# Optimization experiments

Hardware: AMD Instinct MI355X
Metric: run time of the kernel (lower is better)

The kernel has to match this reference:

```python
import jax, jax.numpy as jnp
import numpy as np

LAGS = 2
LATENT = 64          # latent_size; number of tiny per-dim MLPs
HID = 64             # hidden_dim of each MLP2
SLOPE = 0.2          # LeakyReLU negative slope
IN_DIM = LAGS * LATENT + 1  # 129: flattened lags + current value of dim i


def setup_inputs() -> dict:
    key = jax.random.key(0)
    k0, k1, k2, k3, k4 = jax.random.split(key, 5)
    B, LEN = 32, 512
    x = jax.random.normal(k0, (B, LEN + LAGS, LATENT), jnp.float32)
    # Stacked per-latent MLP2 params (num_layers=1):
    #   Linear(IN_DIM -> HID) + LeakyReLU(0.2) + Linear(HID -> 1)
    s1 = float(1.0 / np.sqrt(IN_DIM))
    s2 = float(1.0 / np.sqrt(HID))
    W1 = jax.random.uniform(k1, (LATENT, HID, IN_DIM), jnp.float32, -s1, s1)
    b1 = jax.random.uniform(k2, (LATENT, HID), jnp.float32, -s1, s1)
    W2 = jax.random.uniform(k3, (LATENT, HID), jnp.float32, -s2, s2)
    b2 = jax.random.uniform(k4, (LATENT,), jnp.float32, -s2, s2)
    return {"x": x, "W1": W1, "b1": b1, "W2": W2, "b2": b2}


def reference(x, W1, b1, W2, b2):
    B, T, xd = x.shape
    length = T - LAGS
    N = B * length
    # torch unfold(dim=1, size=LAGS+1, step=1).transpose(2,3) -> [B, length, LAGS+1, xd]
    idx = jnp.arange(length)[:, None] + jnp.arange(LAGS + 1)[None, :]
    win = x[:, idx]                                   # [B, length, LAGS+1, xd]
    lagsx = win[:, :, :-1].reshape(N, LAGS * xd)      # [N, LAGS*xd]
    xt = win[:, :, -1].reshape(N, xd)                 # [N, xd] current values per latent dim
    # gs[i] input = concat(lagsx, xt[:, i:i+1]); batch all latent dims at once.
    W1_lags = W1[:, :, :-1]                           # [L, H, LAGS*xd]
    w1_t = W1[:, :, -1]                               # [L, H] weight on the appended x_t column
    pre = (jnp.einsum('nd,lhd->nlh', lagsx, W1_lags)
           + xt[:, :, None] * w1_t[None]
           + b1[None])                                # [N, L, H]
    act = jnp.where(pre >= 0, pre, SLOPE * pre)       # LeakyReLU(0.2)
    residuals = jnp.einsum('nlh,lh->nl', act, W2) + b2[None]   # [N, L]
    # Analytic last column of the per-sample Jacobian (d residual_i / d x_t_i):
    dact = jnp.where(pre >= 0, 1.0, SLOPE)
    J_last = jnp.einsum('lh,nlh,lh->nl', W2, dact, w1_t)       # [N, L]
    logabsdet = jnp.sum(jnp.log(jnp.abs(J_last)), axis=-1)     # [N]
    return residuals.reshape(B, length, xd), logabsdet.reshape(B, length)
```

## Files before the change

kernel.cpp:

```cpp
#include <hip/hip_runtime.h>
#include <math.h>

#define SLOPE  0.2f
#define NB     32
#define LEN    512
#define LATENT 64
#define HID    64
#define IN_DIM 129
#define TROWS  514
#define NTOT   (NB * LEN)

typedef __attribute__((ext_vector_type(8)))  short bf16x8;
typedef __attribute__((ext_vector_type(16))) float f32x16;
typedef __attribute__((ext_vector_type(4)))  float f32x4;

struct alignas(8) US4 { unsigned short x, y, z, w; };

__device__ inline void bsplit(float v, unsigned short& hi, unsigned short& lo) {
    unsigned int u  = __builtin_bit_cast(unsigned int, v);
    unsigned int hb = (u + 0x7fffu + ((u >> 16) & 1u)) >> 16;
    hi = (unsigned short)hb;
    float fh = __builtin_bit_cast(float, hb << 16);
    float r  = v - fh;
    unsigned int u2 = __builtin_bit_cast(unsigned int, r);
    lo = (unsigned short)((u2 + 0x7fffu + ((u2 >> 16) & 1u)) >> 16);
}

__global__ __launch_bounds__(256)
void conv_w1(const float* __restrict__ W1g, unsigned short* __restrict__ W1f,
             float* __restrict__ W1t, float* __restrict__ out_lad) {
    const int idx = blockIdx.x * 256 + threadIdx.x;
    if (idx < NTOT) out_lad[idx] = 0.f;
    const int row  = idx >> 4;
    const int o    = idx & 15;
    const int ks   = o >> 1, hi32 = o & 1;
    const int l    = row >> 6, h = row & 63;
    const int i    = h >> 5,  r32 = h & 31;
    const int lane = hi32 * 32 + r32;
    const float* src = W1g + (size_t)row * IN_DIM + o * 8;
    unsigned short hh[8], ll[8];
    #pragma unroll
    for (int e = 0; e < 8; ++e) bsplit(src[e], hh[e], ll[e]);
    const size_t base = (size_t)l * 16384 + (size_t)i * 8192 + (size_t)ks * 1024
                      + (size_t)lane * 8;
    *reinterpret_cast<US4*>(W1f + base)       = US4{hh[0], hh[1], hh[2], hh[3]};
    *reinterpret_cast<US4*>(W1f + base + 4)   = US4{hh[4], hh[5], hh[6], hh[7]};
    *reinterpret_cast<US4*>(W1f + base + 512) = US4{ll[0], ll[1], ll[2], ll[3]};
    *reinterpret_cast<US4*>(W1f + base + 516) = US4{ll[4], ll[5], ll[6], ll[7]};
    if (o == 15) W1t[row] = src[8];
}

__global__ __launch_bounds__(512, 2)
void fused_mfma(const float* __restrict__ xg,
                const float* __restrict__ b1g, const float* __restrict__ W2g,
                const float* __restrict__ b2g,
                const unsigned short* __restrict__ W1f,
                const float* __restrict__ W1t,
                float* __restrict__ out_res, float* __restrict__ out_lad)
{
    __shared__ unsigned short sXh[66][72];
    __shared__ unsigned short sXl[66][72];
    __shared__ float sXt[66][8];
    __shared__ float sJ[64][8];
    __shared__ float sR[64][8];

    const int tid  = threadIdx.x;
    const int by   = blockIdx.x & 7;
    const int ht   = blockIdx.x >> 3;
    const int pt   = ht >> 1;
    const int s0   = (ht & 1) * 4;
    const int wn   = tid >> 6;
    const int lane = tid & 63;
    const int r32  = lane & 31;
    const int hi32 = lane >> 5;
    const int l    = by * 8 + wn;

    const unsigned short* A0 = W1f + (size_t)l * 16384 + (size_t)lane * 8;

    #pragma unroll 1
    for (int s = s0; s < s0 + 4; ++s) {
        const size_t xrow0 = (size_t)pt * TROWS + s * 64;

        for (int i = tid; i < 66 * 16; i += 512) {
            const int row = i >> 4, c4 = (i & 15) << 2;
            const float4 v = *reinterpret_cast<const float4*>(
                xg + (xrow0 + row) * LATENT + c4);
            unsigned short h0,h1,h2,h3, l0,l1,l2,l3;
            bsplit(v.x, h0, l0); bsplit(v.y, h1, l1);
            bsplit(v.z, h2, l2); bsplit(v.w, h3, l3);
            *reinterpret_cast<US4*>(&sXh[row][c4]) = US4{h0, h1, h2, h3};
            *reinterpret_cast<US4*>(&sXl[row][c4]) = US4{l0, l1, l2, l3};
        }
        for (int i = tid; i < 66 * 8; i += 512) {
            const int row = i >> 3, w = i & 7;
            sXt[row][w] = xg[(xrow0 + row) * LATENT + by * 8 + w];
        }
        __syncthreads();

        f32x16 acc[2][2];
        #pragma unroll
        for (int i = 0; i < 2; ++i)
            #pragma unroll
            for (int g = 0; g < 4; ++g) {
                const f32x4 b14 = *reinterpret_cast<const f32x4*>(
                    b1g + l * HID + i * 32 + hi32 * 4 + g * 8);
                #pragma unroll
                for (int m = 0; m < 4; ++m) {
                    acc[i][0][g * 4 + m] = b14[m];
                    acc[i][1][g * 4 + m] = b14[m];
                }
            }

        #pragma unroll
        for (int ks = 0; ks < 8; ++ks) {
            const int lag = ks >> 2;
            const int cc  = (ks & 3) * 16 + hi32 * 8;
            const unsigned short* p0 = A0 + ks * 1024;
            bf16x8 awh[2], awl[2], bxh[2], bxl[2];
            #pragma unroll
            for (int i = 0; i < 2; ++i) {
                awh[i] = *reinterpret_cast<const bf16x8*>(p0 + i * 8192);
                awl[i] = *reinterpret_cast<const bf16x8*>(p0 + i * 8192 + 512);
            }
            #pragma unroll
            for (int j = 0; j < 2; ++j) {
                const int rr = j * 32 + r32 + lag;
                bxh[j] = *reinterpret_cast<const bf16x8*>(&sXh[rr][cc]);
                bxl[j] = *reinterpret_cast<const bf16x8*>(&sXl[rr][cc]);
            }
            #pragma unroll
            for (int i = 0; i < 2; ++i)
                #pragma unroll
                for (int j = 0; j < 2; ++j) {
                    acc[i][j] = __builtin_amdgcn_mfma_f32_32x32x16_bf16(awh[i], bxh[j], acc[i][j], 0, 0, 0);
                    acc[i][j] = __builtin_amdgcn_mfma_f32_32x32x16_bf16(awh[i], bxl[j], acc[i][j], 0, 0, 0);
                    acc[i][j] = __builtin_amdgcn_mfma_f32_32x32x16_bf16(awl[i], bxh[j], acc[i][j], 0, 0, 0);
                }
        }

        const float xt0 = sXt[r32 + 2][wn];
        const float xt1 = sXt[32 + r32 + 2][wn];
        float res0 = 0.f, res1 = 0.f, jp0 = 0.f, jp1 = 0.f, jc = 0.f;

        #pragma unroll
        for (int i = 0; i < 2; ++i)
            #pragma unroll
            for (int g = 0; g < 4; ++g) {
                const int h0 = l * HID + i * 32 + hi32 * 4 + g * 8;
                const f32x4 wt = *reinterpret_cast<const f32x4*>(W1t + h0);
                const f32x4 w2 = *reinterpret_cast<const f32x4*>(W2g + h0);
                #pragma unroll
                for (int m = 0; m < 4; ++m) {
                    const float c0 = w2[m] * wt[m];
                    jc += c0;
                    const int r = g * 4 + m;
                    const float pre0 = fmaf(xt0, wt[m], acc[i][0][r]);
                    const float pre1 = fmaf(xt1, wt[m], acc[i][1][r]);
                    res0 += w2[m] * fmaxf(pre0, SLOPE * pre0);
                    res1 += w2[m] * fmaxf(pre1, SLOPE * pre1);
                    jp0 += (pre0 >= 0.f) ? c0 : 0.f;
                    jp1 += (pre1 >= 0.f) ? c0 : 0.f;
                }
            }

        res0 += __shfl_xor(res0, 32);
        res1 += __shfl_xor(res1, 32);
        jp0  += __shfl_xor(jp0, 32);
        jp1  += __shfl_xor(jp1, 32);
        jc   += __shfl_xor(jc, 32);

        if (hi32 == 0) {
            const float b2v = b2g[l];
            sR[r32][wn]      = res0 + b2v;
            sR[r32 + 32][wn] = res1 + b2v;
            sJ[r32][wn]      = SLOPE * jc + (1.f - SLOPE) * jp0;
            sJ[r32 + 32][wn] = SLOPE * jc + (1.f - SLOPE) * jp1;
        }
        __syncthreads();

        const size_t nbase = (size_t)pt * LEN + s * 64;
        if (tid < 128) {
            const int n = tid >> 1, part = (tid & 1) * 4;
            *reinterpret_cast<f32x4*>(out_res + (nbase + n) * LATENT + by * 8 + part) =
                *reinterpret_cast<const f32x4*>(&sR[n][part]);
        } else if (tid >= 448) {
            const int n = tid - 448;
            const float p = sJ[n][0] * sJ[n][1] * sJ[n][2] * sJ[n][3]
                          * sJ[n][4] * sJ[n][5] * sJ[n][6] * sJ[n][7];
            atomicAdd(&out_lad[nbase + n], logf(fabsf(p)));
        }
        __syncthreads();
    }
}

extern "C" void kernel_launch(void* const* d_in, const int* in_sizes, int n_in,
                              void* d_out, int out_size, void* d_ws, size_t ws_size,
                              hipStream_t stream) {
    const float* xg  = (const float*)d_in[0];
    const float* W1g = (const float*)d_in[1];
    const float* b1g = (const float*)d_in[2];
    const float* W2g = (const float*)d_in[3];
    const float* b2g = (const float*)d_in[4];

    float* out_res = (float*)d_out;
    float* out_lad = out_res + (size_t)NTOT * LATENT;

    float*          W1t = (float*)d_ws;
    unsigned short* W1f = (unsigned short*)(W1t + 4096);

    conv_w1<<<256, 256, 0, stream>>>(W1g, W1f, W1t, out_lad);

    dim3 grid(512);
    fused_mfma<<<grid, 512, 0, stream>>>(xg, b1g, W2g, b2g, W1f, W1t,
                                         out_res, out_lad);
}
```

Before: 157.3 us.

## Retile fused MLP kernel: stage 32 rows once, loop over latent dims per block

Each block now stages a 32-sample x tile into shared memory once and then loops over 32 latent dims (4 waves x 8 iterations), instead of staging 64-row tiles four times for a fixed set of 8 latent dims. This cuts repeated x loads and bf16 splitting as well as the per-tile block syncs, and accumulates log|J| in registers with one atomic per block per row. In exchange it reloads W1 fragments from global/L2 for every latent dim. Outputs are written as scattered scalar stores rather than vectorised rows, and the grid grows to 1024 blocks of 256 threads with only one 32-row MFMA tile per wave.

```diff
diff --git a/kernel.cpp b/kernel.cpp
--- a/kernel.cpp
+++ b/kernel.cpp
@@ -50,7 +50,7 @@
     if (o == 15) W1t[row] = src[8];
 }
 
-__global__ __launch_bounds__(512, 2)
+__global__ __launch_bounds__(256, 4)
 void fused_mfma(const float* __restrict__ xg,
                 const float* __restrict__ b1g, const float* __restrict__ W2g,
                 const float* __restrict__ b2g,
@@ -58,90 +58,71 @@
                 const float* __restrict__ W1t,
                 float* __restrict__ out_res, float* __restrict__ out_lad)
 {
-    __shared__ unsigned short sXh[66][72];
-    __shared__ unsigned short sXl[66][72];
-    __shared__ float sXt[66][8];
-    __shared__ float sJ[64][8];
-    __shared__ float sR[64][8];
+    __shared__ unsigned short sXh[34][72];
+    __shared__ unsigned short sXl[34][72];
+    __shared__ float sJ[32][4];
 
-    const int tid  = threadIdx.x;
-    const int by   = blockIdx.x & 7;
-    const int ht   = blockIdx.x >> 3;
-    const int pt   = ht >> 1;
-    const int s0   = (ht & 1) * 4;
+    const int tid   = threadIdx.x;
+    const int tile  = blockIdx.x & 511;
+    const int lhalf = blockIdx.x >> 9;
+    const int pt    = tile >> 4;
+    const int s     = tile & 15;
+    const size_t xrow0 = (size_t)pt * TROWS + s * 32;
+    const size_t nbase = (size_t)tile * 32;
+
+    for (int i = tid; i < 34 * 16; i += 256) {
+        const int row = i >> 4, c4 = (i & 15) << 2;
+        const float4 v = *reinterpret_cast<const float4*>(
+            xg + (xrow0 + row) * LATENT + c4);
+        unsigned short h0,h1,h2,h3, l0,l1,l2,l3;
+        bsplit(v.x, h0, l0); bsplit(v.y, h1, l1);
+        bsplit(v.z, h2, l2); bsplit(v.w, h3, l3);
+        *reinterpret_cast<US4*>(&sXh[row][c4]) = US4{h0, h1, h2, h3};
+        *reinterpret_cast<US4*>(&sXl[row][c4]) = US4{l0, l1, l2, l3};
+    }
+    __syncthreads();
+
     const int wn   = tid >> 6;
     const int lane = tid & 63;
     const int r32  = lane & 31;
     const int hi32 = lane >> 5;
-    const int l    = by * 8 + wn;
 
-    const unsigned short* A0 = W1f + (size_t)l * 16384 + (size_t)lane * 8;
+    float jlog = 0.f, jprod = 1.f;
 
     #pragma unroll 1
-    for (int s = s0; s < s0 + 4; ++s) {
-        const size_t xrow0 = (size_t)pt * TROWS + s * 64;
+    for (int q = 0; q < 8; ++q) {
+        const int l = lhalf * 32 + q * 4 + wn;
+        const unsigned short* A0 = W1f + (size_t)l * 16384 + (size_t)lane * 8;
 
-        for (int i = tid; i < 66 * 16; i += 512) {
-            const int row = i >> 4, c4 = (i & 15) << 2;
-            const float4 v = *reinterpret_cast<const float4*>(
-                xg + (xrow0 + row) * LATENT + c4);
-            unsigned short h0,h1,h2,h3, l0,l1,l2,l3;
-            bsplit(v.x, h0, l0); bsplit(v.y, h1, l1);
-            bsplit(v.z, h2, l2); bsplit(v.w, h3, l3);
-            *reinterpret_cast<US4*>(&sXh[row][c4]) = US4{h0, h1, h2, h3};
-            *reinterpret_cast<US4*>(&sXl[row][c4]) = US4{l0, l1, l2, l3};
-        }
-        for (int i = tid; i < 66 * 8; i += 512) {
-            const int row = i >> 3, w = i & 7;
-            sXt[row][w] = xg[(xrow0 + row) * LATENT + by * 8 + w];
-        }
-        __syncthreads();
-
-        f32x16 acc[2][2];
+        f32x16 acc[2];
         #pragma unroll
         for (int i = 0; i < 2; ++i)
             #pragma unroll
-            for (int g = 0; g < 4; ++g) {
-                const f32x4 b14 = *reinterpret_cast<const f32x4*>(
-                    b1g + l * HID + i * 32 + hi32 * 4 + g * 8);
-                #pragma unroll
-                for (int m = 0; m < 4; ++m) {
-                    acc[i][0][g * 4 + m] = b14[m];
-                    acc[i][1][g * 4 + m] = b14[m];
-                }
-            }
+            for (int r = 0; r < 16; ++r) acc[i][r] = 0.f;
 
         #pragma unroll
         for (int ks = 0; ks < 8; ++ks) {
             const int lag = ks >> 2;
             const int cc  = (ks & 3) * 16 + hi32 * 8;
             const unsigned short* p0 = A0 + ks * 1024;
-            bf16x8 awh[2], awl[2], bxh[2], bxl[2];
+            bf16x8 awh[2], awl[2];
             #pragma unroll
             for (int i = 0; i < 2; ++i) {
                 awh[i] = *reinterpret_cast<const bf16x8*>(p0 + i * 8192);
                 awl[i] = *reinterpret_cast<const bf16x8*>(p0 + i * 8192 + 512);
             }
+            const bf16x8 bxh = *reinterpret_cast<const bf16x8*>(&sXh[r32 + lag][cc]);
+            const bf16x8 bxl = *reinterpret_cast<const bf16x8*>(&sXl[r32 + lag][cc]);
             #pragma unroll
-            for (int j = 0; j < 2; ++j) {
-                const int rr = j * 32 + r32 + lag;
-                bxh[j] = *reinterpret_cast<const bf16x8*>(&sXh[rr][cc]);
-                bxl[j] = *reinterpret_cast<const bf16x8*>(&sXl[rr][cc]);
+            for (int i = 0; i < 2; ++i) {
+                acc[i] = __builtin_amdgcn_mfma_f32_32x32x16_bf16(awh[i], bxh, acc[i], 0, 0, 0);
+                acc[i] = __builtin_amdgcn_mfma_f32_32x32x16_bf16(awh[i], bxl, acc[i], 0, 0, 0);
+                acc[i] = __builtin_amdgcn_mfma_f32_32x32x16_bf16(awl[i], bxh, acc[i], 0, 0, 0);
             }
-            #pragma unroll
-            for (int i = 0; i < 2; ++i)
-                #pragma unroll
-                for (int j = 0; j < 2; ++j) {
-                    acc[i][j] = __builtin_amdgcn_mfma_f32_32x32x16_bf16(awh[i], bxh[j], acc[i][j], 0, 0, 0);
-                    acc[i][j] = __builtin_amdgcn_mfma_f32_32x32x16_bf16(awh[i], bxl[j], acc[i][j], 0, 0, 0);
-                    acc[i][j] = __builtin_amdgcn_mfma_f32_32x32x16_bf16(awl[i], bxh[j], acc[i][j], 0, 0, 0);
-                }
         }
 
-        const float xt0 = sXt[r32 + 2][wn];
-        const float xt1 = sXt[32 + r32 + 2][wn];
-        float res0 = 0.f, res1 = 0.f, jp0 = 0.f, jp1 = 0.f, jc = 0.f;
-
+        const float xt0 = xg[(xrow0 + 2 + r32) * LATENT + l];
+        float res0 = 0.f, jp0 = 0.f, jc = 0.f;
         #pragma unroll
         for (int i = 0; i < 2; ++i)
             #pragma unroll
@@ -149,47 +130,37 @@
                 const int h0 = l * HID + i * 32 + hi32 * 4 + g * 8;
                 const f32x4 wt = *reinterpret_cast<const f32x4*>(W1t + h0);
                 const f32x4 w2 = *reinterpret_cast<const f32x4*>(W2g + h0);
+                const f32x4 b1 = *reinterpret_cast<const f32x4*>(b1g + h0);
                 #pragma unroll
                 for (int m = 0; m < 4; ++m) {
                     const float c0 = w2[m] * wt[m];
                     jc += c0;
-                    const int r = g * 4 + m;
-                    const float pre0 = fmaf(xt0, wt[m], acc[i][0][r]);
-                    const float pre1 = fmaf(xt1, wt[m], acc[i][1][r]);
+                    const float pre0 = fmaf(xt0, wt[m], acc[i][g * 4 + m] + b1[m]);
                     res0 += w2[m] * fmaxf(pre0, SLOPE * pre0);
-                    res1 += w2[m] * fmaxf(pre1, SLOPE * pre1);
                     jp0 += (pre0 >= 0.f) ? c0 : 0.f;
-                    jp1 += (pre1 >= 0.f) ? c0 : 0.f;
                 }
             }
 
         res0 += __shfl_xor(res0, 32);
-        res1 += __shfl_xor(res1, 32);
         jp0  += __shfl_xor(jp0, 32);
-        jp1  += __shfl_xor(jp1, 32);
         jc   += __shfl_xor(jc, 32);
+        const float jac = SLOPE * jc + (1.f - SLOPE) * jp0;
 
-        if (hi32 == 0) {
-            const float b2v = b2g[l];
-            sR[r32][wn]      = res0 + b2v;
-            sR[r32 + 32][wn] = res1 + b2v;
-            sJ[r32][wn]      = SLOPE * jc + (1.f - SLOPE) * jp0;
-            sJ[r32 + 32][wn] = SLOPE * jc + (1.f - SLOPE) * jp1;
+        if (hi32 == 0)
+            out_res[(nbase + r32) * LATENT + l] = res0 + b2g[l];
+
+        jprod *= jac;
+        if ((q & 3) == 3) {
+            jlog += logf(fabsf(jprod));
+            jprod = 1.f;
         }
-        __syncthreads();
+    }
 
-        const size_t nbase = (size_t)pt * LEN + s * 64;
-        if (tid < 128) {
-            const int n = tid >> 1, part = (tid & 1) * 4;
-            *reinterpret_cast<f32x4*>(out_res + (nbase + n) * LATENT + by * 8 + part) =
-                *reinterpret_cast<const f32x4*>(&sR[n][part]);
-        } else if (tid >= 448) {
-            const int n = tid - 448;
-            const float p = sJ[n][0] * sJ[n][1] * sJ[n][2] * sJ[n][3]
-                          * sJ[n][4] * sJ[n][5] * sJ[n][6] * sJ[n][7];
-            atomicAdd(&out_lad[nbase + n], logf(fabsf(p)));
-        }
-        __syncthreads();
+    if (hi32 == 0) sJ[r32][wn] = jlog;
+    __syncthreads();
+    if (tid < 32) {
+        const float part = sJ[tid][0] + sJ[tid][1] + sJ[tid][2] + sJ[tid][3];
+        atomicAdd(&out_lad[nbase + tid], part);
     }
 }
 
@@ -210,7 +181,7 @@
 
     conv_w1<<<256, 256, 0, stream>>>(W1g, W1f, W1t, out_lad);
 
-    dim3 grid(512);
-    fused_mfma<<<grid, 512, 0, stream>>>(xg, b1g, W2g, b2g, W1f, W1t,
+    dim3 grid(1024);
+    fused_mfma<<<grid, 256, 0, stream>>>(xg, b1g, W2g, b2g, W1f, W1t,
                                          out_res, out_lad);
 }
```

After: 143.5 us. -8.8%, faster.
